# Kernel tuning notes

Measured on AMD Instinct MI355X. Metric: run time of the kernel, lower is better.

The kernel has to match this reference:

```python
import jax, jax.numpy as jnp
import numpy as np

EMBED_DIM = 384
B, P, N = 8, 4, 4096


def setup_inputs() -> dict:
    key = jax.random.key(0)
    k1, k2, k3, k4, k5 = jax.random.split(key, 5)
    scale = 1.0 / np.sqrt(EMBED_DIM)
    return {
        "x": jax.random.normal(k1, (B, EMBED_DIM, P, N), dtype=jnp.float32),
        "w_qkv": jax.random.normal(k2, (1 + 2 * EMBED_DIM, EMBED_DIM), dtype=jnp.float32) * scale,
        "b_qkv": jax.random.normal(k3, (1 + 2 * EMBED_DIM,), dtype=jnp.float32) * 0.01,
        "w_out": jax.random.normal(k4, (EMBED_DIM, EMBED_DIM), dtype=jnp.float32) * scale,
        "b_out": jax.random.normal(k5, (EMBED_DIM,), dtype=jnp.float32) * 0.01,
    }


def reference(x, w_qkv, b_qkv, w_out, b_out):
    # x: [B, C, P, N] (C=embed_dim, P=patch area, N=num patches)
    C = x.shape[1]
    # 1x1 conv qkv projection -> [B, 1+2C, P, N]
    qkv = jnp.einsum("bcpn,oc->bopn", x, w_qkv) + b_qkv[None, :, None, None]
    q = qkv[:, :1]            # [B, 1, P, N]
    k = qkv[:, 1:1 + C]       # [B, C, P, N]
    v = qkv[:, 1 + C:]        # [B, C, P, N]
    # softmax over spatial dim N (attn_dropout=0 -> identity)
    context_scores = jax.nn.softmax(q, axis=-1)
    # context vector: weighted sum over N -> [B, C, P, 1]
    context_vector = jnp.sum(k * context_scores, axis=-1, keepdims=True)
    # broadcast-multiply with relu(v)
    out = jax.nn.relu(v) * context_vector
    # 1x1 conv output projection
    out = jnp.einsum("bcpn,oc->bopn", out, w_out) + b_out[None, :, None, None]
    return out
```

## Files before the change

kernel.cpp:

```cpp
#include <hip/hip_runtime.h>
#include <hip/hip_bf16.h>
#include <stdint.h>

#define CC   384
#define BB   8
#define PP   4
#define NNN  4096
#define NBP  32
#define PN   (PP*NNN)

#define AS1 __attribute__((address_space(1)))
#define AS3 __attribute__((address_space(3)))

typedef float  f32x4 __attribute__((ext_vector_type(4)));
typedef short  s16x8 __attribute__((ext_vector_type(8)));
typedef unsigned short u16x4 __attribute__((ext_vector_type(4)));

__device__ __forceinline__ unsigned short f2bf(float f) {
  unsigned int u = __float_as_uint(f);
  u += 0x7fffu + ((u >> 16) & 1u);
  return (unsigned short)(u >> 16);
}
__device__ __forceinline__ float bf2f(unsigned short u) {
  return __uint_as_float(((unsigned int)u) << 16);
}

__device__ __forceinline__ int swz16(int r) {
  return ((r ^ (r >> 2)) & 15) << 4;
}

__device__ __forceinline__ void stage16(const char* g, char* l_uniform, int lane) {
#if defined(__has_builtin) && __has_builtin(__builtin_amdgcn_global_load_lds)
  __builtin_amdgcn_global_load_lds((const AS1 unsigned int*)g,
                                   (AS3 unsigned int*)l_uniform, 16, 0, 0);
#else
  *(int4*)(l_uniform + lane*16) = *(const int4*)g;
#endif
}


__global__ __launch_bounds__(256) void k_pre(
    const float* __restrict__ x, const float* __restrict__ wqkv,
    unsigned short* __restrict__ xbf, float* __restrict__ q)
{
  __shared__ __align__(16) unsigned short tr[24576];
  __shared__ float4 qw[64];
  char* trb = (char*)tr;
  const int bid = blockIdx.x;
  const int bp = bid >> 6, nt = bid & 63;
  const int b = bp >> 2, p = bp & 3;
  const int n0 = nt * 64;
  const int t  = threadIdx.x;
  const int wv_ = t >> 6, lane = t & 63;
  const int cg = t >> 4, nv = t & 15;
  const int r0 = 4 * nv;
  const float* xb = x + (size_t)b*CC*PN + (size_t)p*NNN + n0 + r0;
  const int s0 = swz16(r0+0), s1 = swz16(r0+1), s2 = swz16(r0+2), s3 = swz16(r0+3);

  float4 qa = {0.f, 0.f, 0.f, 0.f};
  #pragma unroll 3
  for (int it = 0; it < 12; ++it) {
    const int c0 = 32*it + 2*cg;
    const float4 x0 = *(const float4*)(xb + (size_t)c0*PN);
    const float4 x1 = *(const float4*)(xb + (size_t)(c0+1)*PN);
    const float w0 = wqkv[c0], w1 = wqkv[c0+1];
    qa.x += w0*x0.x + w1*x1.x;
    qa.y += w0*x0.y + w1*x1.y;
    qa.z += w0*x0.z + w1*x1.z;
    qa.w += w0*x0.w + w1*x1.w;
    const unsigned int p0 = (unsigned)f2bf(x0.x) | ((unsigned)f2bf(x1.x) << 16);
    const unsigned int p1 = (unsigned)f2bf(x0.y) | ((unsigned)f2bf(x1.y) << 16);
    const unsigned int p2 = (unsigned)f2bf(x0.z) | ((unsigned)f2bf(x1.z) << 16);
    const unsigned int p3 = (unsigned)f2bf(x0.w) | ((unsigned)f2bf(x1.w) << 16);
    const int cb = 2*c0;
    *(unsigned int*)(trb + (((r0+0)*768 + cb) ^ s0)) = p0;
    *(unsigned int*)(trb + (((r0+1)*768 + cb) ^ s1)) = p1;
    *(unsigned int*)(trb + (((r0+2)*768 + cb) ^ s2)) = p2;
    *(unsigned int*)(trb + (((r0+3)*768 + cb) ^ s3)) = p3;
  }
  qa.x += __shfl_xor(qa.x, 16); qa.y += __shfl_xor(qa.y, 16);
  qa.z += __shfl_xor(qa.z, 16); qa.w += __shfl_xor(qa.w, 16);
  qa.x += __shfl_xor(qa.x, 32); qa.y += __shfl_xor(qa.y, 32);
  qa.z += __shfl_xor(qa.z, 32); qa.w += __shfl_xor(qa.w, 32);
  if (lane < 16) qw[wv_*16 + lane] = qa;
  __syncthreads();
  const int4* trs = (const int4*)tr;
  int4* dst = (int4*)(xbf + (size_t)bid * 24576);
  #pragma unroll
  for (int j = 0; j < 12; ++j) dst[j*256 + t] = trs[j*256 + t];
  if (t < 16) {
    float4 a0 = qw[t], a1 = qw[16+t], a2 = qw[32+t], a3 = qw[48+t];
    float4 o; o.x = a0.x+a1.x+a2.x+a3.x; o.y = a0.y+a1.y+a2.y+a3.y;
    o.z = a0.z+a1.z+a2.z+a3.z; o.w = a0.w+a1.w+a2.w+a3.w;
    *(float4*)(q + (size_t)bp*NNN + n0 + 4*t) = o;
  }
}

__global__ __launch_bounds__(256) void k_wcvt2(
    const float* __restrict__ wqkv, const float* __restrict__ wout,
    unsigned short* __restrict__ wvt, unsigned short* __restrict__ woutt)
{
  const int i = blockIdx.x*256 + threadIdx.x;
  const int e = (i < CC*CC) ? i : i - CC*CC;
  const int j   = e & 7;
  const int g   = (e >> 3) & 3;
  const int l15 = (e >> 5) & 15;
  const int rem = e >> 9;
  const int ks  = rem % 12;
  const int mf  = rem / 12;
  const int row = 16*mf + l15;
  const int col = 32*ks + 8*g + j;
  if (i < CC*CC) wvt[e]          = f2bf(wqkv[(size_t)(385 + row)*CC + col]);
  else           woutt[e]        = f2bf(wout[(size_t)row*CC + col]);
}

__global__ __launch_bounds__(256) void k_softmax2(
    const float* __restrict__ q, const float* __restrict__ bqkv,
    float* __restrict__ scores)
{
  __shared__ float red[8];
  const int bp = blockIdx.x;
  const int t  = threadIdx.x;
  const int wv_ = t >> 6, ln = t & 63;
  const float bq = bqkv[0];
  float4 qv[4];
  float lmax = -1e30f;
  #pragma unroll
  for (int i = 0; i < 4; ++i) {
    const int n = i*1024 + t*4;
    float4 a = *(const float4*)(q + (size_t)bp*NNN + n);
    qv[i].x = a.x + bq; qv[i].y = a.y + bq; qv[i].z = a.z + bq; qv[i].w = a.w + bq;
    lmax = fmaxf(lmax, fmaxf(fmaxf(qv[i].x, qv[i].y), fmaxf(qv[i].z, qv[i].w)));
  }
  #pragma unroll
  for (int off = 32; off; off >>= 1) lmax = fmaxf(lmax, __shfl_xor(lmax, off));
  if (ln == 0) red[wv_] = lmax;
  __syncthreads();
  const float M = fmaxf(fmaxf(red[0], red[1]), fmaxf(red[2], red[3]));
  float lsum = 0.f;
  #pragma unroll
  for (int i = 0; i < 4; ++i) {
    qv[i].x = expf(qv[i].x - M); qv[i].y = expf(qv[i].y - M);
    qv[i].z = expf(qv[i].z - M); qv[i].w = expf(qv[i].w - M);
    lsum += qv[i].x + qv[i].y + qv[i].z + qv[i].w;
  }
  #pragma unroll
  for (int off = 32; off; off >>= 1) lsum += __shfl_xor(lsum, off);
  if (ln == 0) red[4 + wv_] = lsum;
  __syncthreads();
  const float inv = 1.f / (red[4] + red[5] + red[6] + red[7]);
  #pragma unroll
  for (int i = 0; i < 4; ++i) {
    const int n = i*1024 + t*4;
    float4 o; o.x=qv[i].x*inv; o.y=qv[i].y*inv; o.z=qv[i].z*inv; o.w=qv[i].w*inv;
    *(float4*)(scores + (size_t)bp*NNN + n) = o;
  }
}

__global__ __launch_bounds__(384) void k_xs2(
    const unsigned short* __restrict__ xbf, const float* __restrict__ scores,
    float* __restrict__ partial)
{
  __shared__ __align__(16) char lds[49152];
  __shared__ float sl[64];
  const int bid = blockIdx.x;
  const int bp = bid >> 6, nt = bid & 63;
  const int t = threadIdx.x;
  const int w6 = t >> 6, lane = t & 63;
  const char* gsrc = (const char*)xbf + (size_t)bid * 49152;
  #pragma unroll
  for (int r = 0; r < 8; ++r) {
    const int loff = (r*6 + w6) * 1024;
    stage16(gsrc + loff + lane*16, lds + loff, lane);
  }
  if (t < 64) sl[t] = scores[(size_t)bp*NNN + nt*64 + t];
  __syncthreads();
  float acc = 0.f;
  #pragma unroll 8
  for (int r = 0; r < 64; ++r) {
    const unsigned short uv = *(const unsigned short*)(lds + ((r*768 + 2*t) ^ swz16(r)));
    acc += bf2f(uv) * sl[r];
  }
  partial[(size_t)bid*CC + t] = acc;
}

__global__ __launch_bounds__(384) void k_cv2(
    const float* __restrict__ partial, const float* __restrict__ wqkv,
    const float* __restrict__ bqkv, float* __restrict__ cv)
{
  __shared__ float xsl[CC];
  const int bp = blockIdx.x;
  const int t  = threadIdx.x;
  float s = 0.f;
  #pragma unroll 8
  for (int nt = 0; nt < 64; ++nt) s += partial[((size_t)bp*64 + nt)*CC + t];
  xsl[t] = s;
  __syncthreads();
  float acc = bqkv[1 + t];
  const float* wk = wqkv + (size_t)(1 + t)*CC;
  #pragma unroll 8
  for (int c2 = 0; c2 < CC; ++c2) acc += wk[c2] * xsl[c2];
  cv[(size_t)bp*CC + t] = acc;
}

__device__ __forceinline__ void gemm_t(
    const unsigned short* __restrict__ wt, const char* lds,
    int w, int g, int l15, f32x4 acc[3][4])
{
  const unsigned short* base = wt + (size_t)(3*w)*12*512 + l15*32 + g*8;
  s16x8 a[3][3];
  #pragma unroll
  for (int pf = 0; pf < 3; ++pf)
    #pragma unroll
    for (int mi = 0; mi < 3; ++mi)
      a[pf][mi] = *(const s16x8*)(base + ((size_t)mi*12 + pf)*512);
  #pragma unroll
  for (int ks = 0; ks < 12; ++ks) {
    const int slot = ks % 3;
    s16x8 bfr[4];
    #pragma unroll
    for (int nt = 0; nt < 4; ++nt) {
      const int row = 16*nt + l15;
      const int byteb = (row*768 + 64*ks + 16*g) ^ swz16(row);
      bfr[nt] = *(const s16x8*)(lds + byteb);
    }
    #pragma unroll
    for (int mi = 0; mi < 3; ++mi)
      #pragma unroll
      for (int nt = 0; nt < 4; ++nt)
        acc[mi][nt] = __builtin_amdgcn_mfma_f32_16x16x32_bf16(
            a[slot][mi], bfr[nt], acc[mi][nt], 0, 0, 0);
    if (ks + 3 < 12) {
      #pragma unroll
      for (int mi = 0; mi < 3; ++mi)
        a[slot][mi] = *(const s16x8*)(base + ((size_t)mi*12 + ks + 3)*512);
    }
  }
}

__global__ __launch_bounds__(512, 4) void k_main2(
    const unsigned short* __restrict__ xbf,
    const unsigned short* __restrict__ wvt,
    const unsigned short* __restrict__ woutt,
    const float* __restrict__ cv,
    const float* __restrict__ bqkv,
    const float* __restrict__ bout,
    float* __restrict__ out)
{
  __shared__ __align__(16) char lds[49152];
  const int bid = blockIdx.x;
  const int nb  = bid & 63;
  const int bp  = bid >> 6;
  const int b = bp >> 2, p = bp & 3;
  const int n0 = nb * 64;
  const int tid  = threadIdx.x;
  const int w    = tid >> 6;
  const int lane = tid & 63;
  const int g    = lane >> 4;
  const int l15  = lane & 15;

  {
    const char* gsrc = (const char*)xbf + (size_t)bid * 49152;
    #pragma unroll
    for (int r = 0; r < 6; ++r) {
      const int loff = (r*8 + w) * 1024;
      stage16(gsrc + loff + lane*16, lds + loff, lane);
    }
  }
  __syncthreads();

  f32x4 acc[3][4];
  #pragma unroll
  for (int i = 0; i < 3; ++i)
    #pragma unroll
    for (int j = 0; j < 4; ++j) acc[i][j] = (f32x4){0.f,0.f,0.f,0.f};

  gemm_t(wvt, lds, w, g, l15, acc);
  __syncthreads();

  const float* cvp = cv + (size_t)bp*CC;
  #pragma unroll
  for (int mi = 0; mi < 3; ++mi) {
    const int m0 = 48*w + 16*mi + 4*g;
    const float* bv = bqkv + 385 + m0;
    const float b0 = bv[0], b1 = bv[1], b2 = bv[2], b3 = bv[3];
    const float4 cvv = *(const float4*)(cvp + m0);
    #pragma unroll
    for (int nt = 0; nt < 4; ++nt) {
      const int row = 16*nt + l15;
      const f32x4 t = acc[mi][nt];
      u16x4 pk = { f2bf(fmaxf(t[0]+b0, 0.f)*cvv.x), f2bf(fmaxf(t[1]+b1, 0.f)*cvv.y),
                   f2bf(fmaxf(t[2]+b2, 0.f)*cvv.z), f2bf(fmaxf(t[3]+b3, 0.f)*cvv.w) };
      const int byte0 = (row*768 + 2*m0) ^ swz16(row);
      *(u16x4*)(lds + byte0) = pk;
    }
  }
  __syncthreads();

  #pragma unroll
  for (int i = 0; i < 3; ++i)
    #pragma unroll
    for (int j = 0; j < 4; ++j) acc[i][j] = (f32x4){0.f,0.f,0.f,0.f};

  gemm_t(woutt, lds, w, g, l15, acc);

  float* fl = (float*)lds;
  float* outb = out + (size_t)b*CC*PN + (size_t)p*NNN + n0;
  #pragma unroll
  for (int half = 0; half < 2; ++half) {
    __syncthreads();
    if ((w >> 2) == half) {
      const int wl = w & 3;
      #pragma unroll
      for (int mi = 0; mi < 3; ++mi) {
        const int m0 = 48*w + 16*mi + 4*g;
        const int lr = 48*wl + 16*mi + 4*g;
        const int cs = ((lr >> 2) & 3) << 4;
        const float4 bo = *(const float4*)(bout + m0);
        #pragma unroll
        for (int nt = 0; nt < 4; ++nt) {
          const f32x4 t = acc[mi][nt];
          const int col = (16*nt + l15) ^ cs;
          fl[(lr+0)*64 + col] = t[0] + bo.x;
          fl[(lr+1)*64 + col] = t[1] + bo.y;
          fl[(lr+2)*64 + col] = t[2] + bo.z;
          fl[(lr+3)*64 + col] = t[3] + bo.w;
        }
      }
    }
    __syncthreads();
    #pragma unroll
    for (int ps = 0; ps < 6; ++ps) {
      const int idx = ps*512 + tid;
      const int rr  = idx >> 4;
      const int q4  = (idx & 15) * 4;
      const int cs  = ((rr >> 2) & 3) << 4;
      const float4 v = *(const float4*)(fl + rr*64 + (q4 ^ cs));
      *(float4*)(outb + (size_t)(192*half + rr)*PN + q4) = v;
    }
  }
}


__global__ __launch_bounds__(256) void k_qpart(
    const float* __restrict__ x, const float* __restrict__ wqkv,
    float* __restrict__ qpart)
{
  const int bid = blockIdx.x;
  const int seg = bid & 3;
  const int nc  = (bid >> 2) & 3;
  const int bp  = bid >> 4;
  const int b = bp >> 2, p = bp & 3;
  const int n = nc * 1024 + threadIdx.x * 4;
  const float* xb = x + (size_t)b*CC*PN + (size_t)p*NNN + n;
  float ax = 0.f, ay = 0.f, az = 0.f, aw = 0.f;
  const int c0 = seg * 96;
  #pragma unroll 8
  for (int c = c0; c < c0 + 96; ++c) {
    const float w = wqkv[c];
    const float4 xv = *(const float4*)(xb + (size_t)c*PN);
    ax += w*xv.x; ay += w*xv.y; az += w*xv.z; aw += w*xv.w;
  }
  float4 o; o.x=ax; o.y=ay; o.z=az; o.w=aw;
  *(float4*)(qpart + (size_t)(seg*NBP + bp)*NNN + n) = o;
}

__global__ __launch_bounds__(256) void k_softmax(
    const float* __restrict__ qpart, const float* __restrict__ bqkv,
    float* __restrict__ scores)
{
  __shared__ float red[8];
  const int bp = blockIdx.x;
  const int t  = threadIdx.x;
  const int wv_ = t >> 6, ln = t & 63;
  const float bq = bqkv[0];
  float4 q[4];
  float lmax = -1e30f;
  #pragma unroll
  for (int i = 0; i < 4; ++i) {
    const int n = i*1024 + t*4;
    const float* base = qpart + (size_t)bp*NNN + n;
    const float4 a = *(const float4*)(base);
    const float4 b1 = *(const float4*)(base + (size_t)NBP*NNN);
    const float4 c1 = *(const float4*)(base + (size_t)2*NBP*NNN);
    const float4 d1 = *(const float4*)(base + (size_t)3*NBP*NNN);
    q[i].x = a.x+b1.x+c1.x+d1.x + bq;
    q[i].y = a.y+b1.y+c1.y+d1.y + bq;
    q[i].z = a.z+b1.z+c1.z+d1.z + bq;
    q[i].w = a.w+b1.w+c1.w+d1.w + bq;
    lmax = fmaxf(lmax, fmaxf(fmaxf(q[i].x, q[i].y), fmaxf(q[i].z, q[i].w)));
  }
  #pragma unroll
  for (int off = 32; off; off >>= 1) lmax = fmaxf(lmax, __shfl_xor(lmax, off));
  if (ln == 0) red[wv_] = lmax;
  __syncthreads();
  const float M = fmaxf(fmaxf(red[0], red[1]), fmaxf(red[2], red[3]));
  float lsum = 0.f;
  #pragma unroll
  for (int i = 0; i < 4; ++i) {
    q[i].x = expf(q[i].x - M); q[i].y = expf(q[i].y - M);
    q[i].z = expf(q[i].z - M); q[i].w = expf(q[i].w - M);
    lsum += q[i].x + q[i].y + q[i].z + q[i].w;
  }
  #pragma unroll
  for (int off = 32; off; off >>= 1) lsum += __shfl_xor(lsum, off);
  if (ln == 0) red[4 + wv_] = lsum;
  __syncthreads();
  const float inv = 1.f / (red[4] + red[5] + red[6] + red[7]);
  #pragma unroll
  for (int i = 0; i < 4; ++i) {
    const int n = i*1024 + t*4;
    float4 o; o.x=q[i].x*inv; o.y=q[i].y*inv; o.z=q[i].z*inv; o.w=q[i].w*inv;
    *(float4*)(scores + (size_t)bp*NNN + n) = o;
  }
}

__global__ __launch_bounds__(256) void k_xs(
    const float* __restrict__ x, const float* __restrict__ scores,
    float* __restrict__ xs)
{
  __shared__ float red[4];
  const int c  = blockIdx.x;
  const int bp = blockIdx.y;
  const int b = bp >> 2, p = bp & 3;
  const float* xr = x + ((size_t)b*CC + c)*PN + (size_t)p*NNN;
  const float* sr = scores + (size_t)bp*NNN;
  float acc = 0.f;
  #pragma unroll
  for (int i = 0; i < 4; ++i) {
    const int n = i*1024 + threadIdx.x*4;
    const float4 xv = *(const float4*)(xr + n);
    const float4 sv = *(const float4*)(sr + n);
    acc += xv.x*sv.x + xv.y*sv.y + xv.z*sv.z + xv.w*sv.w;
  }
  #pragma unroll
  for (int off = 32; off; off >>= 1) acc += __shfl_xor(acc, off);
  if ((threadIdx.x & 63) == 0) red[threadIdx.x >> 6] = acc;
  __syncthreads();
  if (threadIdx.x == 0) xs[(size_t)bp*CC + c] = red[0]+red[1]+red[2]+red[3];
}

__global__ __launch_bounds__(256) void k_wcvt(
    const float* __restrict__ wqkv, const float* __restrict__ wout,
    unsigned short* __restrict__ wv, unsigned short* __restrict__ woutb)
{
  const int i = blockIdx.x*256 + threadIdx.x;
  if (i < CC*CC) wv[i] = f2bf(wqkv[385*CC + i]);
  else           woutb[i - CC*CC] = f2bf(wout[i - CC*CC]);
}

__global__ __launch_bounds__(384) void k_cv(
    const float* __restrict__ wqkv, const float* __restrict__ bqkv,
    const float* __restrict__ xs, float* __restrict__ cv)
{
  __shared__ float xsl[CC];
  const int bp = blockIdx.x;
  const int t  = threadIdx.x;
  xsl[t] = xs[(size_t)bp*CC + t];
  __syncthreads();
  float acc = bqkv[1 + t];
  const float* wk = wqkv + (size_t)(1 + t)*CC;
  #pragma unroll 8
  for (int c2 = 0; c2 < CC; ++c2) acc += wk[c2] * xsl[c2];
  cv[(size_t)bp*CC + t] = acc;
}

__device__ __forceinline__ void stage_load(
    const float* __restrict__ xb, int w, int chunk, float s[12])
{
  const int c0 = 96*chunk + 12*w;
  const float* xc = xb + (size_t)c0 * PN;
  #pragma unroll
  for (int k = 0; k < 12; ++k) s[k] = xc[(size_t)k * PN];
}

__device__ __forceinline__ void stage_write(
    char* lds, int w, int n, int chunk, const float s[12])
{
  const int swz = (n & 15) << 4;
  const int c0 = 96*chunk + 12*w;
  #pragma unroll
  for (int j = 0; j < 3; ++j) {
    u16x4 pk = { f2bf(s[4*j]), f2bf(s[4*j+1]), f2bf(s[4*j+2]), f2bf(s[4*j+3]) };
    const int byte0 = (n*768 + 2*(c0 + 4*j)) ^ swz;
    *(u16x4*)(lds + byte0) = pk;
  }
}

template<int KSN>
__device__ __forceinline__ void gemm_ks(
    const unsigned short* __restrict__ wa, const char* lds,
    int w, int g, int l15, int ks0, f32x4 acc[3][4])
{
  const unsigned short* wb = wa + (size_t)(48*w + l15)*CC + 8*g;
  s16x8 afr[2][3];
  #pragma unroll
  for (int mi = 0; mi < 3; ++mi)
    afr[0][mi] = *(const s16x8*)(wb + (size_t)(16*mi)*CC + 32*ks0);
  #pragma unroll
  for (int i = 0; i < KSN; ++i) {
    const int ks  = ks0 + i;
    const int cur = i & 1;
    if (i + 1 < KSN) {
      #pragma unroll
      for (int mi = 0; mi < 3; ++mi)
        afr[cur ^ 1][mi] = *(const s16x8*)(wb + (size_t)(16*mi)*CC + 32*(ks+1));
    }
    s16x8 bfr[4];
    #pragma unroll
    for (int nt = 0; nt < 4; ++nt) {
      const int row = 16*nt + l15;
      const int byteb = (row*768 + 64*ks + 16*g) ^ (l15 << 4);
      bfr[nt] = *(const s16x8*)(lds + byteb);
    }
    #pragma unroll
    for (int mi = 0; mi < 3; ++mi)
      #pragma unroll
      for (int nt = 0; nt < 4; ++nt)
        acc[mi][nt] = __builtin_amdgcn_mfma_f32_16x16x32_bf16(
            afr[cur][mi], bfr[nt], acc[mi][nt], 0, 0, 0);
  }
}

__global__ __launch_bounds__(512, 4) void k_main(
    const float* __restrict__ x,
    const unsigned short* __restrict__ wv,
    const unsigned short* __restrict__ woutb,
    const float* __restrict__ cv,
    const float* __restrict__ bqkv,
    const float* __restrict__ bout,
    float* __restrict__ out)
{
  __shared__ __align__(16) unsigned short lds_u16[64*384];
  char* lds = (char*)lds_u16;
  const int bid = blockIdx.x;
  const int nb  = bid & 63;
  const int bp  = bid >> 6;
  const int b = bp >> 2, p = bp & 3;
  const int n0 = nb * 64;
  const int tid  = threadIdx.x;
  const int w    = tid >> 6;
  const int lane = tid & 63;
  const int g    = lane >> 4;
  const int l15  = lane & 15;

  const float* xb = x + (size_t)b*CC*PN + (size_t)p*NNN + n0 + lane;

  float s[12];
  stage_load(xb, w, 0, s);
  stage_write(lds, w, lane, 0, s);
  stage_load(xb, w, 1, s);
  __syncthreads();

  f32x4 acc[3][4];
  #pragma unroll
  for (int i = 0; i < 3; ++i)
    #pragma unroll
    for (int j = 0; j < 4; ++j) acc[i][j] = (f32x4){0.f,0.f,0.f,0.f};

  for (int c = 0; c < 4; ++c) {
    gemm_ks<3>(wv, lds, w, g, l15, 3*c, acc);
    if (c < 3) {
      stage_write(lds, w, lane, c+1, s);
      if (c < 2) stage_load(xb, w, c+2, s);
    }
    __syncthreads();
  }

  const float* cvp = cv + (size_t)bp*CC;
  #pragma unroll
  for (int mi = 0; mi < 3; ++mi) {
    const int m0 = 48*w + 16*mi + 4*g;
    const float* bv = bqkv + 385 + m0;
    const float b0 = bv[0], b1 = bv[1], b2 = bv[2], b3 = bv[3];
    const float4 cvv = *(const float4*)(cvp + m0);
    #pragma unroll
    for (int nt = 0; nt < 4; ++nt) {
      const int row = 16*nt + l15;
      const f32x4 t = acc[mi][nt];
      u16x4 pk = { f2bf(fmaxf(t[0]+b0, 0.f)*cvv.x), f2bf(fmaxf(t[1]+b1, 0.f)*cvv.y),
                   f2bf(fmaxf(t[2]+b2, 0.f)*cvv.z), f2bf(fmaxf(t[3]+b3, 0.f)*cvv.w) };
      const int byte0 = (row*768 + 2*m0) ^ (l15 << 4);
      *(u16x4*)(lds + byte0) = pk;
    }
  }
  __syncthreads();

  #pragma unroll
  for (int i = 0; i < 3; ++i)
    #pragma unroll
    for (int j = 0; j < 4; ++j) acc[i][j] = (f32x4){0.f,0.f,0.f,0.f};

  gemm_ks<12>(woutb, lds, w, g, l15, 0, acc);

  #pragma unroll
  for (int mi = 0; mi < 3; ++mi) {
    const int m0 = 48*w + 16*mi + 4*g;
    const float4 bo = *(const float4*)(bout + m0);
    #pragma unroll
    for (int nt = 0; nt < 4; ++nt) {
      const int nn = n0 + 16*nt + l15;
      const f32x4 t = acc[mi][nt];
      float* ob = out + ((size_t)b*CC + m0)*PN + (size_t)p*NNN + nn;
      ob[0]            = t[0] + bo.x;
      ob[(size_t)PN]   = t[1] + bo.y;
      ob[2*(size_t)PN] = t[2] + bo.z;
      ob[3*(size_t)PN] = t[3] + bo.w;
    }
  }
}

extern "C" void kernel_launch(void* const* d_in, const int* in_sizes, int n_in,
                              void* d_out, int out_size, void* d_ws, size_t ws_size,
                              hipStream_t stream) {
  const float* x    = (const float*)d_in[0];
  const float* wqkv = (const float*)d_in[1];
  const float* bqkv = (const float*)d_in[2];
  const float* wout = (const float*)d_in[3];
  const float* bout = (const float*)d_in[4];
  float* out = (float*)d_out;
  char* ws = (char*)d_ws;

  const size_t OFF_XBF = 0;
  const size_t OFF_Q   = 100663296;
  const size_t OFF_SC  = 101187584;
  const size_t OFF_PT  = 101711872;
  const size_t OFF_WVT = 104857600;
  const size_t OFF_WOT = 105152512;
  const size_t OFF_CV  = 105447424;
  const size_t NEED    = 105496576;

  if (ws_size >= NEED) {
    unsigned short* xbf   = (unsigned short*)(ws + OFF_XBF);
    float* q              = (float*)(ws + OFF_Q);
    float* scores         = (float*)(ws + OFF_SC);
    float* partial        = (float*)(ws + OFF_PT);
    unsigned short* wvt   = (unsigned short*)(ws + OFF_WVT);
    unsigned short* woutt = (unsigned short*)(ws + OFF_WOT);
    float* cvp            = (float*)(ws + OFF_CV);

    hipLaunchKernelGGL(k_pre,      dim3(2048), dim3(256), 0, stream, x, wqkv, xbf, q);
    hipLaunchKernelGGL(k_wcvt2,    dim3(1152), dim3(256), 0, stream, wqkv, wout, wvt, woutt);
    hipLaunchKernelGGL(k_softmax2, dim3(32),   dim3(256), 0, stream, q, bqkv, scores);
    hipLaunchKernelGGL(k_xs2,      dim3(2048), dim3(384), 0, stream, xbf, scores, partial);
    hipLaunchKernelGGL(k_cv2,      dim3(32),   dim3(384), 0, stream, partial, wqkv, bqkv, cvp);
    hipLaunchKernelGGL(k_main2,    dim3(2048), dim3(512), 0, stream, xbf, wvt, woutt, cvp, bqkv, bout, out);
  } else {
    float* scores         = (float*)(ws);
    float* qpart          = (float*)(ws + 524288);
    float* xs             = (float*)(ws + 2621440);
    unsigned short* wv    = (unsigned short*)(ws + 2719744);
    unsigned short* woutb = (unsigned short*)(ws + 3014656);
    float* cvp            = (float*)(ws + 3309568);

    hipLaunchKernelGGL(k_qpart,   dim3(512),      dim3(256), 0, stream, x, wqkv, qpart);
    hipLaunchKernelGGL(k_wcvt,    dim3(1152),     dim3(256), 0, stream, wqkv, wout, wv, woutb);
    hipLaunchKernelGGL(k_softmax, dim3(32),       dim3(256), 0, stream, qpart, bqkv, scores);
    hipLaunchKernelGGL(k_xs,      dim3(CC, NBP),  dim3(256), 0, stream, x, scores, xs);
    hipLaunchKernelGGL(k_cv,      dim3(NBP),      dim3(384), 0, stream, wqkv, bqkv, xs, cvp);
    hipLaunchKernelGGL(k_main,    dim3(2048),     dim3(512), 0, stream, x, wv, woutb, cvp, bqkv, bout, out);
  }
}
```

Measured before the change: 264.5 us.

## Make main kernel persistent over four tiles with register-resident weights and double-buffered LDS

The main fused kernel now processes four 64-column tiles per block (512 blocks instead of 2048). Each wave keeps its slices of both weight matrices in registers for all tiles, and the next x tile is staged into a second LDS buffer while the current one is computed. Output stores become nontemporal. This removes repeated weight reloads from global memory and overlaps tile loading with MFMA work. The cost is heavy register pressure (72 s16x8 fragments), 144KB of LDS, and one block per CU, which lowers occupancy and may cause spills.

```diff
diff --git a/kernel.cpp b/kernel.cpp
--- a/kernel.cpp
+++ b/kernel.cpp
@@ -203,42 +203,36 @@
   cv[(size_t)bp*CC + t] = acc;
 }
 
-__device__ __forceinline__ void gemm_t(
-    const unsigned short* __restrict__ wt, const char* lds,
-    int w, int g, int l15, f32x4 acc[3][4])
-{
-  const unsigned short* base = wt + (size_t)(3*w)*12*512 + l15*32 + g*8;
-  s16x8 a[3][3];
-  #pragma unroll
-  for (int pf = 0; pf < 3; ++pf)
-    #pragma unroll
-    for (int mi = 0; mi < 3; ++mi)
-      a[pf][mi] = *(const s16x8*)(base + ((size_t)mi*12 + pf)*512);
+__device__ __forceinline__ void stage_tile(const char* gsrc, char* img, int w, int lane) {
+  #pragma unroll
+  for (int r = 0; r < 6; ++r) {
+    const int loff = (r*8 + w) * 1024;
+    stage16(gsrc + loff + lane*16, img + loff, lane);
+  }
+}
+
+__device__ __forceinline__ void gemm_reg(
+    const s16x8 wf[36], const char* ldsb, int g, int l15, f32x4 acc[3][4])
+{
   #pragma unroll
   for (int ks = 0; ks < 12; ++ks) {
-    const int slot = ks % 3;
     s16x8 bfr[4];
     #pragma unroll
     for (int nt = 0; nt < 4; ++nt) {
       const int row = 16*nt + l15;
       const int byteb = (row*768 + 64*ks + 16*g) ^ swz16(row);
-      bfr[nt] = *(const s16x8*)(lds + byteb);
+      bfr[nt] = *(const s16x8*)(ldsb + byteb);
     }
     #pragma unroll
     for (int mi = 0; mi < 3; ++mi)
       #pragma unroll
       for (int nt = 0; nt < 4; ++nt)
         acc[mi][nt] = __builtin_amdgcn_mfma_f32_16x16x32_bf16(
-            a[slot][mi], bfr[nt], acc[mi][nt], 0, 0, 0);
-    if (ks + 3 < 12) {
-      #pragma unroll
-      for (int mi = 0; mi < 3; ++mi)
-        a[slot][mi] = *(const s16x8*)(base + ((size_t)mi*12 + ks + 3)*512);
-    }
-  }
-}
-
-__global__ __launch_bounds__(512, 4) void k_main2(
+            wf[mi*12 + ks], bfr[nt], acc[mi][nt], 0, 0, 0);
+  }
+}
+
+__global__ __launch_bounds__(512, 1) void k_main3(
     const unsigned short* __restrict__ xbf,
     const unsigned short* __restrict__ wvt,
     const unsigned short* __restrict__ woutt,
@@ -247,97 +241,111 @@
     const float* __restrict__ bout,
     float* __restrict__ out)
 {
-  __shared__ __align__(16) char lds[49152];
+  __shared__ __align__(16) char lds[147456];
   const int bid = blockIdx.x;
-  const int nb  = bid & 63;
-  const int bp  = bid >> 6;
+  const int bp  = bid >> 4;
+  const int qt  = bid & 15;
   const int b = bp >> 2, p = bp & 3;
-  const int n0 = nb * 64;
-  const int tid  = threadIdx.x;
-  const int w    = tid >> 6;
-  const int lane = tid & 63;
-  const int g    = lane >> 4;
-  const int l15  = lane & 15;
-
+  const int tid = threadIdx.x;
+  const int w = tid >> 6, lane = tid & 63, g = lane >> 4, l15 = lane & 15;
+  char* const img0 = lds;
+  char* const img1 = lds + 49152;
+  char* const vbuf = lds + 98304;
+
+  s16x8 wvf[36], wof[36];
   {
-    const char* gsrc = (const char*)xbf + (size_t)bid * 49152;
-    #pragma unroll
-    for (int r = 0; r < 6; ++r) {
-      const int loff = (r*8 + w) * 1024;
-      stage16(gsrc + loff + lane*16, lds + loff, lane);
-    }
-  }
-  __syncthreads();
-
-  f32x4 acc[3][4];
-  #pragma unroll
-  for (int i = 0; i < 3; ++i)
-    #pragma unroll
-    for (int j = 0; j < 4; ++j) acc[i][j] = (f32x4){0.f,0.f,0.f,0.f};
-
-  gemm_t(wvt, lds, w, g, l15, acc);
-  __syncthreads();
-
-  const float* cvp = cv + (size_t)bp*CC;
+    const unsigned short* bv = wvt   + (size_t)(36*w)*512 + l15*32 + g*8;
+    const unsigned short* bo = woutt + (size_t)(36*w)*512 + l15*32 + g*8;
+    #pragma unroll
+    for (int i = 0; i < 36; ++i) {
+      wvf[i] = *(const s16x8*)(bv + (size_t)i*512);
+      wof[i] = *(const s16x8*)(bo + (size_t)i*512);
+    }
+  }
+  float4 cvv[3], bvv[3], bov[3];
   #pragma unroll
   for (int mi = 0; mi < 3; ++mi) {
     const int m0 = 48*w + 16*mi + 4*g;
-    const float* bv = bqkv + 385 + m0;
-    const float b0 = bv[0], b1 = bv[1], b2 = bv[2], b3 = bv[3];
-    const float4 cvv = *(const float4*)(cvp + m0);
-    #pragma unroll
-    for (int nt = 0; nt < 4; ++nt) {
-      const int row = 16*nt + l15;
-      const f32x4 t = acc[mi][nt];
-      u16x4 pk = { f2bf(fmaxf(t[0]+b0, 0.f)*cvv.x), f2bf(fmaxf(t[1]+b1, 0.f)*cvv.y),
-                   f2bf(fmaxf(t[2]+b2, 0.f)*cvv.z), f2bf(fmaxf(t[3]+b3, 0.f)*cvv.w) };
-      const int byte0 = (row*768 + 2*m0) ^ swz16(row);
-      *(u16x4*)(lds + byte0) = pk;
-    }
-  }
-  __syncthreads();
-
-  #pragma unroll
-  for (int i = 0; i < 3; ++i)
-    #pragma unroll
-    for (int j = 0; j < 4; ++j) acc[i][j] = (f32x4){0.f,0.f,0.f,0.f};
-
-  gemm_t(woutt, lds, w, g, l15, acc);
-
-  float* fl = (float*)lds;
-  float* outb = out + (size_t)b*CC*PN + (size_t)p*NNN + n0;
-  #pragma unroll
-  for (int half = 0; half < 2; ++half) {
+    cvv[mi] = *(const float4*)(cv + (size_t)bp*CC + m0);
+    bvv[mi] = *(const float4*)(bqkv + 385 + m0);
+    bov[mi] = *(const float4*)(bout + m0);
+  }
+
+  const char* gbase = (const char*)xbf + (size_t)(bid*4) * 49152;
+  stage_tile(gbase, img0, w, lane);
+  __syncthreads();
+
+  #pragma unroll 1
+  for (int j = 0; j < 4; ++j) {
+    char* const imgc = (j & 1) ? img1 : img0;
+    char* const imgn = (j & 1) ? img0 : img1;
+    if (j < 3) stage_tile(gbase + (size_t)(j+1)*49152, imgn, w, lane);
+
+    f32x4 acc[3][4];
+    #pragma unroll
+    for (int i = 0; i < 3; ++i)
+      #pragma unroll
+      for (int k = 0; k < 4; ++k) acc[i][k] = (f32x4){0.f,0.f,0.f,0.f};
+
+    gemm_reg(wvf, imgc, g, l15, acc);
+
+    #pragma unroll
+    for (int mi = 0; mi < 3; ++mi) {
+      const int cb = 2*(48*w + 16*mi + 4*g);
+      #pragma unroll
+      for (int nt = 0; nt < 4; ++nt) {
+        const int row = 16*nt + l15;
+        const f32x4 t = acc[mi][nt];
+        u16x4 pk = { f2bf(fmaxf(t[0]+bvv[mi].x, 0.f)*cvv[mi].x),
+                     f2bf(fmaxf(t[1]+bvv[mi].y, 0.f)*cvv[mi].y),
+                     f2bf(fmaxf(t[2]+bvv[mi].z, 0.f)*cvv[mi].z),
+                     f2bf(fmaxf(t[3]+bvv[mi].w, 0.f)*cvv[mi].w) };
+        *(u16x4*)(vbuf + ((row*768 + cb) ^ swz16(row))) = pk;
+      }
+    }
     __syncthreads();
-    if ((w >> 2) == half) {
-      const int wl = w & 3;
+
+    #pragma unroll
+    for (int i = 0; i < 3; ++i)
       #pragma unroll
-      for (int mi = 0; mi < 3; ++mi) {
-        const int m0 = 48*w + 16*mi + 4*g;
-        const int lr = 48*wl + 16*mi + 4*g;
-        const int cs = ((lr >> 2) & 3) << 4;
-        const float4 bo = *(const float4*)(bout + m0);
+      for (int k = 0; k < 4; ++k) acc[i][k] = (f32x4){0.f,0.f,0.f,0.f};
+
+    gemm_reg(wof, vbuf, g, l15, acc);
+
+    float* fl = (float*)imgc;
+    float* outb = out + (size_t)b*CC*PN + (size_t)p*NNN + (qt*4 + j)*64;
+    #pragma unroll
+    for (int half = 0; half < 2; ++half) {
+      __syncthreads();
+      if ((w >> 2) == half) {
+        const int wl = w & 3;
         #pragma unroll
-        for (int nt = 0; nt < 4; ++nt) {
-          const f32x4 t = acc[mi][nt];
-          const int col = (16*nt + l15) ^ cs;
-          fl[(lr+0)*64 + col] = t[0] + bo.x;
-          fl[(lr+1)*64 + col] = t[1] + bo.y;
-          fl[(lr+2)*64 + col] = t[2] + bo.z;
-          fl[(lr+3)*64 + col] = t[3] + bo.w;
+        for (int mi = 0; mi < 3; ++mi) {
+          const int lr = 48*wl + 16*mi + 4*g;
+          const int cs = g << 4;
+          #pragma unroll
+          for (int nt = 0; nt < 4; ++nt) {
+            const f32x4 t = acc[mi][nt];
+            const int col = (16*nt + l15) ^ cs;
+            fl[(lr+0)*64 + col] = t[0] + bov[mi].x;
+            fl[(lr+1)*64 + col] = t[1] + bov[mi].y;
+            fl[(lr+2)*64 + col] = t[2] + bov[mi].z;
+            fl[(lr+3)*64 + col] = t[3] + bov[mi].w;
+          }
         }
       }
+      __syncthreads();
+      #pragma unroll
+      for (int ps = 0; ps < 6; ++ps) {
+        const int idx = ps*512 + tid;
+        const int rr  = idx >> 4;
+        const int q4  = (idx & 15) * 4;
+        const int cs  = ((rr >> 2) & 3) << 4;
+        const f32x4 v = *(const f32x4*)(fl + rr*64 + (q4 ^ cs));
+        __builtin_nontemporal_store(v, (f32x4*)(outb + (size_t)(192*half + rr)*PN + q4));
+      }
     }
     __syncthreads();
-    #pragma unroll
-    for (int ps = 0; ps < 6; ++ps) {
-      const int idx = ps*512 + tid;
-      const int rr  = idx >> 4;
-      const int q4  = (idx & 15) * 4;
-      const int cs  = ((rr >> 2) & 3) << 4;
-      const float4 v = *(const float4*)(fl + rr*64 + (q4 ^ cs));
-      *(float4*)(outb + (size_t)(192*half + rr)*PN + q4) = v;
-    }
   }
 }
 
@@ -644,7 +652,7 @@
     hipLaunchKernelGGL(k_softmax2, dim3(32),   dim3(256), 0, stream, q, bqkv, scores);
     hipLaunchKernelGGL(k_xs2,      dim3(2048), dim3(384), 0, stream, xbf, scores, partial);
     hipLaunchKernelGGL(k_cv2,      dim3(32),   dim3(384), 0, stream, partial, wqkv, bqkv, cvp);
-    hipLaunchKernelGGL(k_main2,    dim3(2048), dim3(512), 0, stream, xbf, wvt, woutt, cvp, bqkv, bout, out);
+    hipLaunchKernelGGL(k_main3,    dim3(512),  dim3(512), 0, stream, xbf, wvt, woutt, cvp, bqkv, bout, out);
   } else {
     float* scores         = (float*)(ws);
     float* qpart          = (float*)(ws + 524288);
```

Result: slower. 409.9 us (+54.9%).

## Make main kernel persistent over four tiles with double-buffered LDS prefetch

Applied to the files above, without the earlier changes.

The main fused GEMM kernel now processes four consecutive 64-column tiles per block (512 blocks instead of 2048). It uses two 48KB LDS images so the next tile's bf16 input is staged while the current tile runs both GEMMs. The output transpose through LDS is also changed to write all 8 waves' results in two 32-column halves. The goal is to hide global-load latency behind MFMA work and amortize block setup. In exchange, LDS doubles to 96KB per block, which caps occupancy at fewer blocks per CU, and only 512 blocks remain to fill the GPU.

```diff
diff --git a/kernel.cpp b/kernel.cpp
--- a/kernel.cpp
+++ b/kernel.cpp
@@ -203,6 +203,14 @@
   cv[(size_t)bp*CC + t] = acc;
 }
 
+__device__ __forceinline__ void stage_tile(const char* gsrc, char* img, int w, int lane) {
+  #pragma unroll
+  for (int r = 0; r < 6; ++r) {
+    const int loff = (r*8 + w) * 1024;
+    stage16(gsrc + loff + lane*16, img + loff, lane);
+  }
+}
+
 __device__ __forceinline__ void gemm_t(
     const unsigned short* __restrict__ wt, const char* lds,
     int w, int g, int l15, f32x4 acc[3][4])
@@ -238,7 +246,7 @@
   }
 }
 
-__global__ __launch_bounds__(512, 4) void k_main2(
+__global__ __launch_bounds__(512, 2) void k_main4(
     const unsigned short* __restrict__ xbf,
     const unsigned short* __restrict__ wvt,
     const unsigned short* __restrict__ woutt,
@@ -247,97 +255,89 @@
     const float* __restrict__ bout,
     float* __restrict__ out)
 {
-  __shared__ __align__(16) char lds[49152];
+  __shared__ __align__(16) char lds[98304];
   const int bid = blockIdx.x;
-  const int nb  = bid & 63;
-  const int bp  = bid >> 6;
+  const int bp  = bid >> 4;
   const int b = bp >> 2, p = bp & 3;
-  const int n0 = nb * 64;
-  const int tid  = threadIdx.x;
-  const int w    = tid >> 6;
-  const int lane = tid & 63;
-  const int g    = lane >> 4;
-  const int l15  = lane & 15;
-
-  {
-    const char* gsrc = (const char*)xbf + (size_t)bid * 49152;
-    #pragma unroll
-    for (int r = 0; r < 6; ++r) {
-      const int loff = (r*8 + w) * 1024;
-      stage16(gsrc + loff + lane*16, lds + loff, lane);
-    }
-  }
-  __syncthreads();
-
-  f32x4 acc[3][4];
-  #pragma unroll
-  for (int i = 0; i < 3; ++i)
-    #pragma unroll
-    for (int j = 0; j < 4; ++j) acc[i][j] = (f32x4){0.f,0.f,0.f,0.f};
-
-  gemm_t(wvt, lds, w, g, l15, acc);
-  __syncthreads();
-
+  const int tid = threadIdx.x;
+  const int w = tid >> 6, lane = tid & 63, g = lane >> 4, l15 = lane & 15;
   const float* cvp = cv + (size_t)bp*CC;
-  #pragma unroll
-  for (int mi = 0; mi < 3; ++mi) {
-    const int m0 = 48*w + 16*mi + 4*g;
-    const float* bv = bqkv + 385 + m0;
-    const float b0 = bv[0], b1 = bv[1], b2 = bv[2], b3 = bv[3];
-    const float4 cvv = *(const float4*)(cvp + m0);
-    #pragma unroll
-    for (int nt = 0; nt < 4; ++nt) {
-      const int row = 16*nt + l15;
-      const f32x4 t = acc[mi][nt];
-      u16x4 pk = { f2bf(fmaxf(t[0]+b0, 0.f)*cvv.x), f2bf(fmaxf(t[1]+b1, 0.f)*cvv.y),
-                   f2bf(fmaxf(t[2]+b2, 0.f)*cvv.z), f2bf(fmaxf(t[3]+b3, 0.f)*cvv.w) };
-      const int byte0 = (row*768 + 2*m0) ^ swz16(row);
-      *(u16x4*)(lds + byte0) = pk;
-    }
-  }
-  __syncthreads();
-
-  #pragma unroll
-  for (int i = 0; i < 3; ++i)
-    #pragma unroll
-    for (int j = 0; j < 4; ++j) acc[i][j] = (f32x4){0.f,0.f,0.f,0.f};
-
-  gemm_t(woutt, lds, w, g, l15, acc);
-
-  float* fl = (float*)lds;
-  float* outb = out + (size_t)b*CC*PN + (size_t)p*NNN + n0;
-  #pragma unroll
-  for (int half = 0; half < 2; ++half) {
+
+  const char* gbase = (const char*)xbf + (size_t)(bid*4) * 49152;
+  stage_tile(gbase, lds, w, lane);
+  __syncthreads();
+
+  #pragma unroll 1
+  for (int j = 0; j < 4; ++j) {
+    char* const imgc = lds + (j & 1) * 49152;
+    char* const imgn = lds + ((j & 1) ^ 1) * 49152;
+    if (j < 3) stage_tile(gbase + (size_t)(j+1)*49152, imgn, w, lane);
+
+    f32x4 acc[3][4];
+    #pragma unroll
+    for (int i = 0; i < 3; ++i)
+      #pragma unroll
+      for (int k = 0; k < 4; ++k) acc[i][k] = (f32x4){0.f,0.f,0.f,0.f};
+
+    gemm_t(wvt, imgc, w, g, l15, acc);
     __syncthreads();
-    if ((w >> 2) == half) {
-      const int wl = w & 3;
+
+    #pragma unroll
+    for (int mi = 0; mi < 3; ++mi) {
+      const int m0 = 48*w + 16*mi + 4*g;
+      const float* bv = bqkv + 385 + m0;
+      const float b0 = bv[0], b1 = bv[1], b2 = bv[2], b3 = bv[3];
+      const float4 cvv = *(const float4*)(cvp + m0);
+      #pragma unroll
+      for (int nt = 0; nt < 4; ++nt) {
+        const int row = 16*nt + l15;
+        const f32x4 t = acc[mi][nt];
+        u16x4 pk = { f2bf(fmaxf(t[0]+b0, 0.f)*cvv.x), f2bf(fmaxf(t[1]+b1, 0.f)*cvv.y),
+                     f2bf(fmaxf(t[2]+b2, 0.f)*cvv.z), f2bf(fmaxf(t[3]+b3, 0.f)*cvv.w) };
+        const int byte0 = (row*768 + 2*m0) ^ swz16(row);
+        *(u16x4*)(imgc + byte0) = pk;
+      }
+    }
+    __syncthreads();
+
+    #pragma unroll
+    for (int i = 0; i < 3; ++i)
+      #pragma unroll
+      for (int k = 0; k < 4; ++k) acc[i][k] = (f32x4){0.f,0.f,0.f,0.f};
+
+    gemm_t(woutt, imgc, w, g, l15, acc);
+
+    float* fl = (float*)imgc;
+    const int n0 = ((bid & 15)*4 + j) * 64;
+    float* outb = out + (size_t)b*CC*PN + (size_t)p*NNN + n0;
+    #pragma unroll
+    for (int half = 0; half < 2; ++half) {
+      __syncthreads();
       #pragma unroll
       for (int mi = 0; mi < 3; ++mi) {
         const int m0 = 48*w + 16*mi + 4*g;
-        const int lr = 48*wl + 16*mi + 4*g;
-        const int cs = ((lr >> 2) & 3) << 4;
         const float4 bo = *(const float4*)(bout + m0);
         #pragma unroll
-        for (int nt = 0; nt < 4; ++nt) {
-          const f32x4 t = acc[mi][nt];
-          const int col = (16*nt + l15) ^ cs;
-          fl[(lr+0)*64 + col] = t[0] + bo.x;
-          fl[(lr+1)*64 + col] = t[1] + bo.y;
-          fl[(lr+2)*64 + col] = t[2] + bo.z;
-          fl[(lr+3)*64 + col] = t[3] + bo.w;
+        for (int nt2 = 0; nt2 < 2; ++nt2) {
+          const f32x4 t = acc[mi][2*half + nt2];
+          const int colh = 16*nt2 + l15;
+          fl[(m0+0)*32 + colh] = t[0] + bo.x;
+          fl[(m0+1)*32 + colh] = t[1] + bo.y;
+          fl[(m0+2)*32 + colh] = t[2] + bo.z;
+          fl[(m0+3)*32 + colh] = t[3] + bo.w;
         }
       }
+      __syncthreads();
+      #pragma unroll
+      for (int ps = 0; ps < 6; ++ps) {
+        const int idx = ps*512 + tid;
+        const int row = idx >> 3;
+        const int nq  = idx & 7;
+        const float4 v = *(const float4*)(fl + row*32 + nq*4);
+        *(float4*)(outb + (size_t)row*PN + 32*half + nq*4) = v;
+      }
     }
     __syncthreads();
-    #pragma unroll
-    for (int ps = 0; ps < 6; ++ps) {
-      const int idx = ps*512 + tid;
-      const int rr  = idx >> 4;
-      const int q4  = (idx & 15) * 4;
-      const int cs  = ((rr >> 2) & 3) << 4;
-      const float4 v = *(const float4*)(fl + rr*64 + (q4 ^ cs));
-      *(float4*)(outb + (size_t)(192*half + rr)*PN + q4) = v;
-    }
   }
 }
 
@@ -644,7 +644,7 @@
     hipLaunchKernelGGL(k_softmax2, dim3(32),   dim3(256), 0, stream, q, bqkv, scores);
     hipLaunchKernelGGL(k_xs2,      dim3(2048), dim3(384), 0, stream, xbf, scores, partial);
     hipLaunchKernelGGL(k_cv2,      dim3(32),   dim3(384), 0, stream, partial, wqkv, bqkv, cvp);
-    hipLaunchKernelGGL(k_main2,    dim3(2048), dim3(512), 0, stream, xbf, wvt, woutt, cvp, bqkv, bout, out);
+    hipLaunchKernelGGL(k_main4,    dim3(512),  dim3(512), 0, stream, xbf, wvt, woutt, cvp, bqkv, bout, out);
   } else {
     float* scores         = (float*)(ws);
     float* qpart          = (float*)(ws + 524288);
```

After: 525.4 us. 1.99x slower.
